# Kernel tuning notes

Measured on AMD Instinct MI355X. Metric: run time of the kernel, lower is better.

## Reference

```python
import jax, jax.numpy as jnp
import numpy as np

N_NODES = 65536
IN_DIM = 512
OUT_DIM = 512
N_EDGES = 524288
BN_EPS = 1e-5
NORM_EPS = 1e-6


def setup_inputs() -> dict:
    key = jax.random.key(0)
    k1, k2, k3, k4 = jax.random.split(key, 4)
    features = jax.random.normal(k1, (N_NODES, IN_DIM), dtype=jnp.float32)
    edge_index = jax.random.randint(k2, (2, N_EDGES), 0, N_NODES, dtype=jnp.int64)
    # torch Linear weight layout: [out_features, in_features] with in = 2*IN_DIM
    W = jax.random.normal(k3, (OUT_DIM, 2 * IN_DIM), dtype=jnp.float32) * (1.0 / np.sqrt(2 * IN_DIM))
    b = jax.random.normal(k4, (OUT_DIM,), dtype=jnp.float32) * 0.01
    gamma = jnp.ones((OUT_DIM,), dtype=jnp.float32)
    beta = jnp.zeros((OUT_DIM,), dtype=jnp.float32)
    running_mean = jnp.zeros((OUT_DIM,), dtype=jnp.float32)
    running_var = jnp.ones((OUT_DIM,), dtype=jnp.float32)
    return {
        "features": features,
        "edge_index": edge_index,
        "W": W,
        "b": b,
        "gamma": gamma,
        "beta": beta,
        "running_mean": running_mean,
        "running_var": running_var,
    }


def reference(features, edge_index, W, b, gamma, beta, running_mean, running_var):
    sources = edge_index[0]
    targets = edge_index[1]
    # scatter-sum of neighbor (target) features into source rows  [N, D]
    aggregated = jax.ops.segment_sum(features[targets], sources, num_segments=N_NODES)
    out = jnp.concatenate([features, aggregated], axis=1)  # [N, 2D]
    out = out @ W.T + b  # [N, OUT_DIM]
    out = jax.nn.relu(out)
    # BatchNorm1d (eval mode, running stats)
    out = (out - running_mean) * jax.lax.rsqrt(running_var + BN_EPS) * gamma + beta
    # dropout is identity in inference
    out = out / (jnp.linalg.norm(out, axis=1, keepdims=True) + NORM_EPS)
    return out
```

## Files before the change

kernel.cpp:

```cpp
#include <hip/hip_runtime.h>
#include <hip/hip_bf16.h>

#define N_NODES 65536
#define DIM 512
#define N_EDGES 524288
#define BN_EPS 1e-5f
#define NORM_EPS 1e-6f

typedef __attribute__((ext_vector_type(8))) short short8;
typedef __attribute__((ext_vector_type(4))) float f32x4;

static __device__ __forceinline__ unsigned f2bf(float f) {
    union { float f; unsigned u; } c; c.f = f;
    unsigned u = c.u;
    return (u + 0x7fffu + ((u >> 16) & 1u)) >> 16;
}
static __device__ __forceinline__ float bf16lo(unsigned u) {
    union { unsigned u; float f; } c; c.u = u << 16; return c.f;
}
static __device__ __forceinline__ float bf16hi(unsigned u) {
    union { unsigned u; float f; } c; c.u = u & 0xffff0000u; return c.f;
}
static __device__ __forceinline__ uint4 pack8(float4 a, float4 b) {
    uint4 o;
    o.x = f2bf(a.x) | (f2bf(a.y) << 16);
    o.y = f2bf(a.z) | (f2bf(a.w) << 16);
    o.z = f2bf(b.x) | (f2bf(b.y) << 16);
    o.w = f2bf(b.z) | (f2bf(b.w) << 16);
    return o;
}

__global__ void convert_kernel(const float* __restrict__ src,
                               unsigned short* __restrict__ dst, int n8) {
    int i = blockIdx.x * blockDim.x + threadIdx.x;
    if (i < n8) {
        const float4* s = (const float4*)src + i * 2;
        float4 f0 = s[0], f1 = s[1];
        ((uint4*)dst)[i] = pack8(f0, f1);
    }
}

__global__ void hist_kernel(const int* __restrict__ src, int* __restrict__ counts) {
    int e = blockIdx.x * blockDim.x + threadIdx.x;
    if (e < N_EDGES) atomicAdd(&counts[src[e]], 1);
}

__global__ void scan_partial(const int* __restrict__ counts, int* __restrict__ partials) {
    __shared__ int ws[4];
    int t = threadIdx.x;
    int v = counts[blockIdx.x * 256 + t];
#pragma unroll
    for (int d = 1; d < 64; d <<= 1) v += __shfl_xor(v, d);
    if ((t & 63) == 0) ws[t >> 6] = v;
    __syncthreads();
    if (t == 0) partials[blockIdx.x] = ws[0] + ws[1] + ws[2] + ws[3];
}

__global__ void scan_base(int* __restrict__ partials) {
    __shared__ int lds[256];
    int t = threadIdx.x;
    int v = partials[t];
    lds[t] = v;
    __syncthreads();
    for (int d = 1; d < 256; d <<= 1) {
        int mine = lds[t];
        int add = (t >= d) ? lds[t - d] : 0;
        __syncthreads();
        lds[t] = mine + add;
        __syncthreads();
    }
    partials[t] = lds[t] - v;
}

__global__ void scan_final(const int* __restrict__ counts,
                           const int* __restrict__ partials,
                           int* __restrict__ offsets, int* __restrict__ cursor) {
    __shared__ int lds[256];
    int t = threadIdx.x, b = blockIdx.x;
    int v = counts[b * 256 + t];
    lds[t] = v;
    __syncthreads();
    for (int d = 1; d < 256; d <<= 1) {
        int mine = lds[t];
        int add = (t >= d) ? lds[t - d] : 0;
        __syncthreads();
        lds[t] = mine + add;
        __syncthreads();
    }
    int excl = lds[t] - v + partials[b];
    offsets[b * 256 + t] = excl;
    cursor[b * 256 + t] = excl;
    if (b == 255 && t == 255) offsets[N_NODES] = excl + v;
}

__global__ void scatter_kernel(const int* __restrict__ src, const int* __restrict__ tgt,
                               int* __restrict__ cursor, int* __restrict__ sortedT) {
    int e = blockIdx.x * blockDim.x + threadIdx.x;
    if (e < N_EDGES) {
        int s = src[e];
        int pos = atomicAdd(&cursor[s], 1);
        sortedT[pos] = tgt[e];
    }
}

__global__ void aggregate_kernel(const unsigned short* __restrict__ Xb,
                                 const int* __restrict__ offsets,
                                 const int* __restrict__ sortedT,
                                 unsigned short* __restrict__ agg) {
    int wave = (blockIdx.x * blockDim.x + threadIdx.x) >> 6;
    int lane = threadIdx.x & 63;
    if (wave >= N_NODES) return;
    int beg = offsets[wave], end = offsets[wave + 1];
    float a[8] = {0.f, 0.f, 0.f, 0.f, 0.f, 0.f, 0.f, 0.f};
    const uint4* F = (const uint4*)Xb;
    for (int i = beg; i < end; ++i) {
        int t = sortedT[i];
        uint4 v = F[t * 64 + lane];
        a[0] += bf16lo(v.x); a[1] += bf16hi(v.x);
        a[2] += bf16lo(v.y); a[3] += bf16hi(v.y);
        a[4] += bf16lo(v.z); a[5] += bf16hi(v.z);
        a[6] += bf16lo(v.w); a[7] += bf16hi(v.w);
    }
    uint4 o;
    o.x = f2bf(a[0]) | (f2bf(a[1]) << 16);
    o.y = f2bf(a[2]) | (f2bf(a[3]) << 16);
    o.z = f2bf(a[4]) | (f2bf(a[5]) << 16);
    o.w = f2bf(a[6]) | (f2bf(a[7]) << 16);
    ((uint4*)agg)[wave * 64 + lane] = o;
}

__global__ __launch_bounds__(256) void gemm_kernel(
        const unsigned short* __restrict__ Xb,
        const unsigned short* __restrict__ agg,
        const unsigned short* __restrict__ Wb,
        const float* __restrict__ bias,
        const float* __restrict__ gamma,
        const float* __restrict__ beta,
        const float* __restrict__ rmean,
        const float* __restrict__ rvar,
        float* __restrict__ out) {
    __shared__ uint4 Alds[1024];
    __shared__ uint4 Blds[1024];

    const int t = threadIdx.x;
    const int n0 = blockIdx.x * 128;
    const int m0 = blockIdx.y * 128;
    const int w = t >> 6, L = t & 63;
    const int wm = (w >> 1) * 64, wn = (w & 1) * 64;
    const int ml = L & 15, quad = L >> 4;

    f32x4 acc[4][4];
#pragma unroll
    for (int mi = 0; mi < 4; ++mi)
#pragma unroll
        for (int ni = 0; ni < 4; ++ni)
            acc[mi][ni] = (f32x4){0.f, 0.f, 0.f, 0.f};

    for (int kt = 0; kt < 16; ++kt) {
        const unsigned short* Asrc = (kt < 8) ? (Xb + kt * 64) : (agg + (kt - 8) * 64);
        const unsigned short* Bsrc = Wb + kt * 64;
        __syncthreads();
#pragma unroll
        for (int i = 0; i < 4; ++i) {
            int c = i * 256 + t;
            int r = c >> 3, pp = c & 7;
            int p = pp ^ (r & 7);
            const unsigned short* ga = Asrc + (m0 + r) * 512 + p * 8;
            const unsigned short* gb = Bsrc + (n0 + r) * 1024 + p * 8;
            char* la = (char*)Alds + (i * 256 + (t & 192)) * 16;
            char* lb = (char*)Blds + (i * 256 + (t & 192)) * 16;
            __builtin_amdgcn_global_load_lds(
                (const __attribute__((address_space(1))) unsigned int*)ga,
                (__attribute__((address_space(3))) unsigned int*)la, 16, 0, 0);
            __builtin_amdgcn_global_load_lds(
                (const __attribute__((address_space(1))) unsigned int*)gb,
                (__attribute__((address_space(3))) unsigned int*)lb, 16, 0, 0);
        }
        __syncthreads();
#pragma unroll
        for (int kc = 0; kc < 2; ++kc) {
            int g = kc * 4 + quad;
            short8 a[4], b[4];
#pragma unroll
            for (int mi = 0; mi < 4; ++mi) {
                int ra = wm + mi * 16 + ml;
                a[mi] = *(const short8*)&Alds[ra * 8 + (g ^ (ra & 7))];
                int rb = wn + mi * 16 + ml;
                b[mi] = *(const short8*)&Blds[rb * 8 + (g ^ (rb & 7))];
            }
#pragma unroll
            for (int mi = 0; mi < 4; ++mi)
#pragma unroll
                for (int ni = 0; ni < 4; ++ni)
                    acc[mi][ni] = __builtin_amdgcn_mfma_f32_16x16x32_bf16(
                        a[mi], b[ni], acc[mi][ni], 0, 0, 0);
        }
    }

#pragma unroll
    for (int ni = 0; ni < 4; ++ni) {
        int col = n0 + wn + ni * 16 + ml;
        float bi = bias[col];
        float sc = gamma[col] * __frsqrt_rn(rvar[col] + BN_EPS);
        float sh = beta[col] - rmean[col] * sc;
#pragma unroll
        for (int mi = 0; mi < 4; ++mi) {
#pragma unroll
            for (int r = 0; r < 4; ++r) {
                int m = m0 + wm + mi * 16 + quad * 4 + r;
                float v = acc[mi][ni][r] + bi;
                v = fmaxf(v, 0.f) * sc + sh;
                out[m * 512 + col] = v;
            }
        }
    }
}

__global__ void normalize_kernel(float* __restrict__ out) {
    int wave = (blockIdx.x * blockDim.x + threadIdx.x) >> 6;
    int lane = threadIdx.x & 63;
    if (wave >= N_NODES) return;
    float4* O = (float4*)out;
    int base = wave * 128 + lane * 2;
    float4 v0 = O[base], v1 = O[base + 1];
    float ss = v0.x * v0.x + v0.y * v0.y + v0.z * v0.z + v0.w * v0.w
             + v1.x * v1.x + v1.y * v1.y + v1.z * v1.z + v1.w * v1.w;
#pragma unroll
    for (int d = 1; d < 64; d <<= 1) ss += __shfl_xor(ss, d);
    float inv = 1.f / (sqrtf(ss) + NORM_EPS);
    v0.x *= inv; v0.y *= inv; v0.z *= inv; v0.w *= inv;
    v1.x *= inv; v1.y *= inv; v1.z *= inv; v1.w *= inv;
    O[base] = v0;
    O[base + 1] = v1;
}

extern "C" void kernel_launch(void* const* d_in, const int* in_sizes, int n_in,
                              void* d_out, int out_size, void* d_ws, size_t ws_size,
                              hipStream_t stream) {
    const float* features = (const float*)d_in[0];
    const int* edges      = (const int*)d_in[1];
    const float* W        = (const float*)d_in[2];
    const float* bias     = (const float*)d_in[3];
    const float* gamma    = (const float*)d_in[4];
    const float* beta     = (const float*)d_in[5];
    const float* rmean    = (const float*)d_in[6];
    const float* rvar     = (const float*)d_in[7];
    float* out = (float*)d_out;

    char* ws = (char*)d_ws;
    int* counts   = (int*)(ws);
    int* offsets  = (int*)(ws + 0x100000);
    int* cursor   = (int*)(ws + 0x200000);
    int* partials = (int*)(ws + 0x280000);
    int* sortedT  = (int*)(ws + 0x300000);
    unsigned short* Wb  = (unsigned short*)(ws + 0x500000);
    unsigned short* Xb  = (unsigned short*)(ws + 0x600000);
    unsigned short* agg = (unsigned short*)(ws + 0x4600000);

    const int* src = edges;
    const int* tgt = edges + N_EDGES;

    hipMemsetAsync(counts, 0, N_NODES * sizeof(int), stream);
    hist_kernel<<<N_EDGES / 256, 256, 0, stream>>>(src, counts);
    scan_partial<<<256, 256, 0, stream>>>(counts, partials);
    scan_base<<<1, 256, 0, stream>>>(partials);
    scan_final<<<256, 256, 0, stream>>>(counts, partials, offsets, cursor);
    scatter_kernel<<<N_EDGES / 256, 256, 0, stream>>>(src, tgt, cursor, sortedT);
    convert_kernel<<<(N_NODES * DIM / 8) / 256, 256, 0, stream>>>(features, Xb, N_NODES * DIM / 8);
    convert_kernel<<<(DIM * 2 * DIM / 8) / 256, 256, 0, stream>>>(W, Wb, DIM * 2 * DIM / 8);
    aggregate_kernel<<<N_NODES / 4, 256, 0, stream>>>(Xb, offsets, sortedT, agg);
    dim3 grid_gemm(4, N_NODES / 128);
    gemm_kernel<<<grid_gemm, 256, 0, stream>>>(Xb, agg, Wb, bias, gamma, beta,
                                               rmean, rvar, out);
    normalize_kernel<<<N_NODES / 4, 256, 0, stream>>>(out);
}
```

Measured before the change: 512.6 us.

## Fuse row L2 normalization into GEMM epilogue with full-width output tiles

The GEMM is retiled so each 512-thread block computes a 64-row by full 512-column output tile, with each of 8 waves owning 64 columns. Row sums of squares are reduced through shuffles and shared memory, so the L2 normalization is applied before the single store and the separate normalize kernel is removed. This avoids a full read and rewrite of the 128 MB fp32 output. The trade-off is that the whole 512-column slice of W (64 KB per k-step) is reloaded into LDS by every block, and A-tile reuse across columns is lower.

```diff
diff --git a/kernel.cpp b/kernel.cpp
--- a/kernel.cpp
+++ b/kernel.cpp
@@ -129,7 +129,7 @@
     ((uint4*)agg)[wave * 64 + lane] = o;
 }
 
-__global__ __launch_bounds__(256) void gemm_kernel(
+__global__ __launch_bounds__(512, 4) void fused_gemm_norm_kernel(
         const unsigned short* __restrict__ Xb,
         const unsigned short* __restrict__ agg,
         const unsigned short* __restrict__ Wb,
@@ -139,15 +139,15 @@
         const float* __restrict__ rmean,
         const float* __restrict__ rvar,
         float* __restrict__ out) {
-    __shared__ uint4 Alds[1024];
-    __shared__ uint4 Blds[1024];
+    __shared__ uint4 Alds[512];
+    __shared__ uint4 Blds[4096];
+    __shared__ float ssm[64][8];
 
     const int t = threadIdx.x;
-    const int n0 = blockIdx.x * 128;
-    const int m0 = blockIdx.y * 128;
+    const int m0 = blockIdx.x * 64;
     const int w = t >> 6, L = t & 63;
-    const int wm = (w >> 1) * 64, wn = (w & 1) * 64;
     const int ml = L & 15, quad = L >> 4;
+    const int wn = w * 64;
 
     f32x4 acc[4][4];
 #pragma unroll
@@ -158,20 +158,24 @@
 
     for (int kt = 0; kt < 16; ++kt) {
         const unsigned short* Asrc = (kt < 8) ? (Xb + kt * 64) : (agg + (kt - 8) * 64);
-        const unsigned short* Bsrc = Wb + kt * 64;
-        __syncthreads();
-#pragma unroll
-        for (int i = 0; i < 4; ++i) {
-            int c = i * 256 + t;
+        __syncthreads();
+        {
+            int c = t;
             int r = c >> 3, pp = c & 7;
             int p = pp ^ (r & 7);
             const unsigned short* ga = Asrc + (m0 + r) * 512 + p * 8;
-            const unsigned short* gb = Bsrc + (n0 + r) * 1024 + p * 8;
-            char* la = (char*)Alds + (i * 256 + (t & 192)) * 16;
-            char* lb = (char*)Blds + (i * 256 + (t & 192)) * 16;
+            char* la = (char*)Alds + (t & 448) * 16;
             __builtin_amdgcn_global_load_lds(
                 (const __attribute__((address_space(1))) unsigned int*)ga,
                 (__attribute__((address_space(3))) unsigned int*)la, 16, 0, 0);
+        }
+#pragma unroll
+        for (int j = 0; j < 8; ++j) {
+            int c = j * 512 + t;
+            int r = c >> 3, pp = c & 7;
+            int p = pp ^ (r & 7);
+            const unsigned short* gb = Wb + r * 1024 + kt * 64 + p * 8;
+            char* lb = (char*)Blds + (j * 512 + (t & 448)) * 16;
             __builtin_amdgcn_global_load_lds(
                 (const __attribute__((address_space(1))) unsigned int*)gb,
                 (__attribute__((address_space(3))) unsigned int*)lb, 16, 0, 0);
@@ -183,7 +187,7 @@
             short8 a[4], b[4];
 #pragma unroll
             for (int mi = 0; mi < 4; ++mi) {
-                int ra = wm + mi * 16 + ml;
+                int ra = mi * 16 + ml;
                 a[mi] = *(const short8*)&Alds[ra * 8 + (g ^ (ra & 7))];
                 int rb = wn + mi * 16 + ml;
                 b[mi] = *(const short8*)&Blds[rb * 8 + (g ^ (rb & 7))];
@@ -197,41 +201,60 @@
         }
     }
 
+    float bi[4], sc[4], sh[4];
 #pragma unroll
     for (int ni = 0; ni < 4; ++ni) {
-        int col = n0 + wn + ni * 16 + ml;
-        float bi = bias[col];
-        float sc = gamma[col] * __frsqrt_rn(rvar[col] + BN_EPS);
-        float sh = beta[col] - rmean[col] * sc;
-#pragma unroll
-        for (int mi = 0; mi < 4; ++mi) {
+        int col = wn + ni * 16 + ml;
+        bi[ni] = bias[col];
+        sc[ni] = gamma[col] * __frsqrt_rn(rvar[col] + BN_EPS);
+        sh[ni] = beta[col] - rmean[col] * sc[ni];
+    }
+    float ss[4][4];
+#pragma unroll
+    for (int mi = 0; mi < 4; ++mi)
+#pragma unroll
+        for (int r = 0; r < 4; ++r)
+            ss[mi][r] = 0.f;
+#pragma unroll
+    for (int mi = 0; mi < 4; ++mi)
+#pragma unroll
+        for (int ni = 0; ni < 4; ++ni)
 #pragma unroll
             for (int r = 0; r < 4; ++r) {
-                int m = m0 + wm + mi * 16 + quad * 4 + r;
-                float v = acc[mi][ni][r] + bi;
-                v = fmaxf(v, 0.f) * sc + sh;
-                out[m * 512 + col] = v;
+                float v = fmaxf(acc[mi][ni][r] + bi[ni], 0.f) * sc[ni] + sh[ni];
+                acc[mi][ni][r] = v;
+                ss[mi][r] += v * v;
             }
-        }
-    }
-}
-
-__global__ void normalize_kernel(float* __restrict__ out) {
-    int wave = (blockIdx.x * blockDim.x + threadIdx.x) >> 6;
-    int lane = threadIdx.x & 63;
-    if (wave >= N_NODES) return;
-    float4* O = (float4*)out;
-    int base = wave * 128 + lane * 2;
-    float4 v0 = O[base], v1 = O[base + 1];
-    float ss = v0.x * v0.x + v0.y * v0.y + v0.z * v0.z + v0.w * v0.w
-             + v1.x * v1.x + v1.y * v1.y + v1.z * v1.z + v1.w * v1.w;
-#pragma unroll
-    for (int d = 1; d < 64; d <<= 1) ss += __shfl_xor(ss, d);
-    float inv = 1.f / (sqrtf(ss) + NORM_EPS);
-    v0.x *= inv; v0.y *= inv; v0.z *= inv; v0.w *= inv;
-    v1.x *= inv; v1.y *= inv; v1.z *= inv; v1.w *= inv;
-    O[base] = v0;
-    O[base + 1] = v1;
+#pragma unroll
+    for (int mi = 0; mi < 4; ++mi)
+#pragma unroll
+        for (int r = 0; r < 4; ++r) {
+#pragma unroll
+            for (int d = 1; d < 16; d <<= 1)
+                ss[mi][r] += __shfl_xor(ss[mi][r], d);
+        }
+    if (ml == 0) {
+#pragma unroll
+        for (int mi = 0; mi < 4; ++mi)
+#pragma unroll
+            for (int r = 0; r < 4; ++r)
+                ssm[mi * 16 + quad * 4 + r][w] = ss[mi][r];
+    }
+    __syncthreads();
+#pragma unroll
+    for (int mi = 0; mi < 4; ++mi)
+#pragma unroll
+        for (int r = 0; r < 4; ++r) {
+            int rl = mi * 16 + quad * 4 + r;
+            const float4* sp = (const float4*)ssm[rl];
+            float4 s0 = sp[0], s1 = sp[1];
+            float tot = s0.x + s0.y + s0.z + s0.w + s1.x + s1.y + s1.z + s1.w;
+            float inv = 1.f / (sqrtf(tot) + NORM_EPS);
+            int m = m0 + rl;
+#pragma unroll
+            for (int ni = 0; ni < 4; ++ni)
+                out[m * 512 + wn + ni * 16 + ml] = acc[mi][ni][r] * inv;
+        }
 }
 
 extern "C" void kernel_launch(void* const* d_in, const int* in_sizes, int n_in,
@@ -269,8 +292,6 @@
     convert_kernel<<<(N_NODES * DIM / 8) / 256, 256, 0, stream>>>(features, Xb, N_NODES * DIM / 8);
     convert_kernel<<<(DIM * 2 * DIM / 8) / 256, 256, 0, stream>>>(W, Wb, DIM * 2 * DIM / 8);
     aggregate_kernel<<<N_NODES / 4, 256, 0, stream>>>(Xb, offsets, sortedT, agg);
-    dim3 grid_gemm(4, N_NODES / 128);
-    gemm_kernel<<<grid_gemm, 256, 0, stream>>>(Xb, agg, Wb, bias, gamma, beta,
-                                               rmean, rvar, out);
-    normalize_kernel<<<N_NODES / 4, 256, 0, stream>>>(out);
-}
+    fused_gemm_norm_kernel<<<N_NODES / 64, 512, 0, stream>>>(
+        Xb, agg, Wb, bias, gamma, beta, rmean, rvar, out);
+}
```

New measurement: 451.4 us. -12.0%, faster.
